# Optimization experiments

Measured on AMD Instinct MI355X. Metric: run time of the kernel, lower is better.

## Reference

```python
import jax, jax.numpy as jnp
import numpy as np

H, W, C = 384, 384, 200
HIDE, CNN_OUT, NCLS = 128, 64, 16
N = H * W
E = 1179648
EPS = 1e-5  # torch BatchNorm eps


def _bn(x, g, b, axes):
    # training-mode batch norm (biased variance), matches torch BN in train mode
    m = x.mean(axes, keepdims=True)
    v = x.var(axes, keepdims=True)
    return (x - m) * jax.lax.rsqrt(v + EPS) * g + b


def _gcn(x, w, bias, src, dst, n):
    # PyG GCNConv: add self loops, symmetric D^-1/2 (A+I) D^-1/2 normalization
    h = x @ w  # [N, out]
    loop = jnp.arange(n, dtype=src.dtype)
    s = jnp.concatenate([src, loop])
    d = jnp.concatenate([dst, loop])
    deg = jax.ops.segment_sum(jnp.ones(s.shape, x.dtype), d, num_segments=n)
    dinv = jnp.where(deg > 0, jax.lax.rsqrt(jnp.maximum(deg, 1.0)) * (deg > 0), 0.0)
    norm = dinv[s] * dinv[d]  # [E+N]
    out = jax.ops.segment_sum(h[s] * norm[:, None], d, num_segments=n)
    return out + bias


def _gnn_layer(x, bn_g, bn_b, w, b, src, dst):
    # F.normalize (row L2) -> BN1d -> GCNConv -> LeakyReLU (dropout off in eval)
    nrm = jnp.linalg.norm(x, axis=1, keepdims=True)
    x = x / jnp.maximum(nrm, 1e-12)
    x = _bn(x, bn_g, bn_b, (0,))
    return jax.nn.leaky_relu(_gcn(x, w, b, src, dst, x.shape[0]))


def setup_inputs() -> dict:
    key = jax.random.key(0)
    ks = jax.random.split(key, 16)
    p = {}
    p["x"] = jax.random.normal(ks[0], (H, W, C), jnp.float32)
    p["edge_index"] = jax.random.randint(ks[1], (2, E), 0, N, jnp.int32)
    # CNN_denoise: BN(C) -> 1x1 conv C->128 -> BN(128) -> 1x1 conv 128->128
    p["dn_bn1_g"] = jnp.ones((C,), jnp.float32); p["dn_bn1_b"] = jnp.zeros((C,), jnp.float32)
    p["dn_w1"] = jax.random.normal(ks[2], (C, HIDE), jnp.float32) * 0.05
    p["dn_b1"] = jnp.zeros((HIDE,), jnp.float32)
    p["dn_bn2_g"] = jnp.ones((HIDE,), jnp.float32); p["dn_bn2_b"] = jnp.zeros((HIDE,), jnp.float32)
    p["dn_w2"] = jax.random.normal(ks[3], (HIDE, HIDE), jnp.float32) * 0.05
    p["dn_b2"] = jnp.zeros((HIDE,), jnp.float32)
    # CNNCONV(128,64,k=5): BN(128) -> point 1x1 128->64 (no bias) -> depthwise 5x5 (bias)
    p["cnn_bn_g"] = jnp.ones((HIDE,), jnp.float32); p["cnn_bn_b"] = jnp.zeros((HIDE,), jnp.float32)
    p["cnn_pw"] = jax.random.normal(ks[4], (HIDE, CNN_OUT), jnp.float32) * 0.05
    p["cnn_dw"] = jax.random.normal(ks[5], (CNN_OUT, 1, 5, 5), jnp.float32) * 0.05
    p["cnn_db"] = jnp.zeros((CNN_OUT,), jnp.float32)
    # GCN branch: GNN(128,128), GNN(128,128), GNN(128,64)
    dims = [(HIDE, HIDE), (HIDE, HIDE), (HIDE, CNN_OUT)]
    for i, (di, do) in enumerate(dims, 1):
        p[f"g{i}_bn_g"] = jnp.ones((di,), jnp.float32)
        p[f"g{i}_bn_b"] = jnp.zeros((di,), jnp.float32)
        p[f"g{i}_w"] = jax.random.normal(ks[5 + i], (di, do), jnp.float32) * 0.05
        p[f"g{i}_b"] = jnp.zeros((do,), jnp.float32)
    p["lin_w"] = jax.random.normal(ks[9], (HIDE, NCLS), jnp.float32) * 0.05
    p["lin_b"] = jnp.zeros((NCLS,), jnp.float32)
    return p


def reference(x, edge_index,
              dn_bn1_g, dn_bn1_b, dn_w1, dn_b1, dn_bn2_g, dn_bn2_b, dn_w2, dn_b2,
              cnn_bn_g, cnn_bn_b, cnn_pw, cnn_dw, cnn_db,
              g1_bn_g, g1_bn_b, g1_w, g1_b,
              g2_bn_g, g2_bn_b, g2_w, g2_b,
              g3_bn_g, g3_bn_b, g3_w, g3_b,
              lin_w, lin_b):
    src, dst = edge_index[0], edge_index[1]
    # CNN_denoise (channel-last; 1x1 convs are matmuls)
    h = _bn(x, dn_bn1_g, dn_bn1_b, (0, 1))
    h = jax.nn.leaky_relu(h @ dn_w1 + dn_b1)
    h = _bn(h, dn_bn2_g, dn_bn2_b, (0, 1))
    clean = jax.nn.leaky_relu(h @ dn_w2 + dn_b2)       # [H,W,128]
    flat = clean.reshape(N, HIDE)
    # CNN branch: BN -> 1x1 -> LeakyReLU -> depthwise 5x5 -> LeakyReLU
    c = _bn(clean, cnn_bn_g, cnn_bn_b, (0, 1))
    c = jax.nn.leaky_relu(c @ cnn_pw)                  # [H,W,64]
    cn = c.transpose(2, 0, 1)[None]                    # [1,64,H,W]
    cn = jax.lax.conv_general_dilated(
        cn, cnn_dw, (1, 1), 'SAME', feature_group_count=CNN_OUT,
        dimension_numbers=('NCHW', 'OIHW', 'NCHW'))
    cn = jax.nn.leaky_relu(cn[0].transpose(1, 2, 0) + cnn_db)
    cnn_res = cn.reshape(N, CNN_OUT)
    # GCN branch (3 layers)
    g = _gnn_layer(flat, g1_bn_g, g1_bn_b, g1_w, g1_b, src, dst)
    g = _gnn_layer(g, g2_bn_g, g2_bn_b, g2_w, g2_b, src, dst)
    g = _gnn_layer(g, g3_bn_g, g3_bn_b, g3_w, g3_b, src, dst)
    y = jnp.concatenate([g, cnn_res], axis=-1) @ lin_w + lin_b
    return jax.nn.softmax(y, axis=-1)
```

## Files before the change

kernel.cpp:

```cpp
#include <hip/hip_runtime.h>
#include <stddef.h>

#define HH 384
#define WW 384
#define CC 200
#define NN 147456
#define EE 1179648
#define HIDE 128
#define COUT 64
#define NCLS 16
#define BN_EPS 1e-5f

#define SREP 16
#define SLOTF (512 * SREP)
#define DBINS 64

#define NBKT 72
#define NPBK 288
#define EPB  4096

using u16 = unsigned short;
typedef __attribute__((ext_vector_type(8))) short short8;
typedef __attribute__((ext_vector_type(4))) float float4v;

__device__ __forceinline__ float b2f(u16 u) {
    union { unsigned int i; float f; } v; v.i = ((unsigned int)u) << 16; return v.f;
}
__device__ __forceinline__ u16 f2b(float f) {
    union { float f; unsigned int i; } v; v.f = f;
    unsigned int x = v.i;
    unsigned int r = (x + 0x7fffu + ((x >> 16) & 1u)) >> 16;
    return (u16)r;
}
__device__ __forceinline__ float lrelu(float v) { return v > 0.f ? v : 0.01f * v; }

__device__ __forceinline__ void gload_lds16(const void* g, void* l) {
    __builtin_amdgcn_global_load_lds(
        (const __attribute__((address_space(1))) void*)g,
        (__attribute__((address_space(3))) void*)l, 16, 0, 0);
}

__global__ void sniff(const u16* __restrict__ x, int* __restrict__ flag) {
    __shared__ int cntS;
    if (threadIdx.x == 0) cntS = 0;
    __syncthreads();
    int c = 0;
    for (int i = 0; i < 8; i++) {
        u16 h = x[threadIdx.x * 8 + i];
        int hb = (h >> 8) & 0x7F;
        if (hb >= 0x3C && hb <= 0x41) c++;
    }
    atomicAdd(&cntS, c);
    __syncthreads();
    if (threadIdx.x == 0) *flag = (cntS < 1536) ? 1 : 0;
}

#define NPAR 27
struct PConv { const void* src[NPAR]; int n[NPAR]; int off[NPAR]; };

__global__ void convert_params(PConv pc, const int* __restrict__ flag,
                               u16* __restrict__ dst) {
    int b = blockIdx.x;
    int n = pc.n[b];
    const void* s = pc.src[b];
    u16* d = dst + pc.off[b];
    int isf = *flag;
    if (isf) {
        const float* sf = (const float*)s;
        for (int i = threadIdx.x; i < n; i += 256) d[i] = f2b(sf[i]);
    } else {
        const u16* sh = (const u16*)s;
        for (int i = threadIdx.x; i < n; i += 256) d[i] = sh[i];
    }
}

__global__ __launch_bounds__(256) void stats200(const void* __restrict__ X,
                                                const int* __restrict__ flag,
                                                float* __restrict__ arena) {
    __shared__ __align__(16) u16 s[128 * 200];
    int t = threadIdx.x;
    int r0 = blockIdx.x * 128;
    if (*flag) {
        const float* Xf = (const float*)X;
        for (int i = t; i < 128 * 25; i += 256) {
            int r = i / 25, kc = i - r * 25;
            const float* p = Xf + (size_t)(r0 + r) * CC + kc * 8;
            float4v a = *(const float4v*)p;
            float4v b = *(const float4v*)(p + 4);
            short8 v;
            #pragma unroll
            for (int j = 0; j < 4; j++) { v[j] = (short)f2b(a[j]); v[4 + j] = (short)f2b(b[j]); }
            *(short8*)&s[r * 200 + kc * 8] = v;
        }
    } else {
        const u16* Xh = (const u16*)X;
        for (int i = t; i < 128 * 25; i += 256) {
            int r = i / 25, kc = i - r * 25;
            *(short8*)&s[r * 200 + kc * 8] =
                *(const short8*)(Xh + (size_t)(r0 + r) * CC + kc * 8);
        }
    }
    __syncthreads();
    if (t < CC) {
        float sum = 0.f, sq = 0.f;
        for (int r = 0; r < 128; r++) {
            float v = b2f(s[r * 200 + t]);
            sum += v; sq += v * v;
        }
        float* rep = arena + (blockIdx.x & (SREP - 1)) * 512;
        atomicAdd(&rep[t], sum);
        atomicAdd(&rep[256 + t], sq);
    }
}

template<int K, int KPAD, int O>
__global__ __launch_bounds__(256) void fold_bn(
        const float* __restrict__ arena, float invN,
        const u16* __restrict__ bng, const u16* __restrict__ bnb,
        const u16* __restrict__ Wsrc, const u16* __restrict__ extrab,
        u16* __restrict__ WT, float* __restrict__ cb) {
    __shared__ float aS[KPAD], sS[KPAD];
    int t = threadIdx.x;
    if (t < KPAD) {
        float a = 0.f, sh = 0.f;
        if (t < K) {
            float sum = 0.f, sq = 0.f;
            #pragma unroll
            for (int r = 0; r < SREP; r++) {
                sum += arena[r * 512 + t];
                sq  += arena[r * 512 + 256 + t];
            }
            float m = sum * invN;
            float var = fmaxf(sq * invN - m * m, 0.f);
            a = b2f(bng[t]) * rsqrtf(var + BN_EPS);
            sh = b2f(bnb[t]) - m * a;
        }
        aS[t] = a; sS[t] = sh;
    }
    __syncthreads();
    int g = t >> 6, l = t & 63;
    int o = blockIdx.x * 4 + g;
    if (o < O) {
        float c = 0.f;
        #pragma unroll
        for (int k = l; k < KPAD; k += 64) {
            float w = (k < K) ? b2f(Wsrc[k * O + o]) : 0.f;
            c += sS[k] * w;
            WT[o * KPAD + k] = f2b(aS[k] * w);
        }
        #pragma unroll
        for (int s = 32; s >= 1; s >>= 1) c += __shfl_down(c, s);
        if (l == 0) cb[o] = c + (extrab ? b2f(extrab[o]) : 0.f);
    }
}

template<int KT, int KSRC, int O, bool LEAKY, bool SCALE, int STATS, bool DUAL>
__global__ __launch_bounds__(256) void gemm_mfma(
        const void* __restrict__ Ap, const u16* __restrict__ WT,
        const float* __restrict__ cb, const float* __restrict__ s1,
        const float* __restrict__ s2, const int* __restrict__ f32p,
        u16* __restrict__ out, float* __restrict__ stA,
        float* __restrict__ stB, float* __restrict__ invn,
        u16* __restrict__ out2, const u16* __restrict__ zpad) {
    constexpr int KPAD = KT * 32;
    constexpr int CHD = KSRC / 8;
    constexpr int ROWCH = ((KT * 4 + 7) / 8) * 8;
    constexpr int ROWE = ROWCH * 8;
    constexpr int LPR = ROWCH;
    constexpr int RPI = 64 / LPR;
    constexpr int NSI = 64 / RPI;
    constexpr int NCT = O / 16;
    constexpr int CPW = NCT / 4;
    __shared__ __align__(16) u16 As[64 * ROWE];
    __shared__ float rS[4][64];
    __shared__ float invS[64];
    __shared__ float sS1[64], sS2[64];
    int tid = threadIdx.x;
    int row0 = blockIdx.x * 64;

    int isf = f32p ? *f32p : 0;
    if (isf) {
        const float* A = (const float*)Ap;
        for (int i = tid; i < 64 * ROWCH; i += 256) {
            int r = i / ROWCH, slot = i - r * ROWCH;
            int chunk = slot ^ (r & 7);
            short8 v = {0, 0, 0, 0, 0, 0, 0, 0};
            if (chunk < CHD) {
                const float* p = A + (size_t)(row0 + r) * KSRC + chunk * 8;
                float4v a = *(const float4v*)p;
                float4v b = *(const float4v*)(p + 4);
                #pragma unroll
                for (int j = 0; j < 4; j++) { v[j] = (short)f2b(a[j]); v[4 + j] = (short)f2b(b[j]); }
            }
            *(short8*)&As[r * ROWE + slot * 8] = v;
        }
    } else {
        const u16* A = (const u16*)Ap;
        int l = tid & 63, wv = tid >> 6;
        int rl0 = l / LPR, cL = l - rl0 * LPR;
        #pragma unroll
        for (int s = 0; s < NSI / 4; s++) {
            int si = wv + s * 4;
            int rL = si * RPI + rl0;
            int chunk = cL ^ (rL & 7);
            const u16* src = (chunk < CHD)
                ? A + (size_t)(row0 + rL) * KSRC + chunk * 8 : zpad;
            gload_lds16(src, (char*)As + si * 1024);
        }
    }
    if (SCALE && tid < 64) { sS1[tid] = s1[row0 + tid]; sS2[tid] = s2[row0 + tid]; }
    __syncthreads();

    int w = tid >> 6, lane = tid & 63, m = lane & 15, q = lane >> 4;
    float4v acc[4][CPW];
    #pragma unroll
    for (int mf = 0; mf < 4; mf++)
        #pragma unroll
        for (int cp = 0; cp < CPW; cp++)
            acc[mf][cp] = (float4v){0.f, 0.f, 0.f, 0.f};

    const u16* Bbp = WT + (size_t)((w * CPW) * 16 + m) * KPAD + q * 8;

    #pragma unroll
    for (int kt = 0; kt < KT; kt++) {
        short8 af[4];
        int slot = (kt * 4 + q) ^ (m & 7);
        #pragma unroll
        for (int mf = 0; mf < 4; mf++)
            af[mf] = *(const short8*)&As[(size_t)(mf * 16 + m) * ROWE + slot * 8];
        #pragma unroll
        for (int cp = 0; cp < CPW; cp++) {
            short8 bf = *(const short8*)(Bbp + (size_t)cp * 16 * KPAD + kt * 32);
            #pragma unroll
            for (int mf = 0; mf < 4; mf++)
                acc[mf][cp] = __builtin_amdgcn_mfma_f32_16x16x32_bf16(
                    af[mf], bf, acc[mf][cp], 0, 0, 0);
        }
    }

    float rp[4][4] = {};
    #pragma unroll
    for (int cp = 0; cp < CPW; cp++) {
        int ct = w * CPW + cp;
        int col = ct * 16 + m;
        float cbv = cb[col];
        #pragma unroll
        for (int mf = 0; mf < 4; mf++) {
            #pragma unroll
            for (int r = 0; r < 4; r++) {
                int rl = mf * 16 + q * 4 + r;
                float x = acc[mf][cp][r];
                if constexpr (DUAL) {
                    if (ct < 8) {
                        x = (x * sS1[rl] + cbv) * sS2[rl];
                        out[(size_t)(row0 + rl) * 128 + col] = f2b(x);
                    } else {
                        x = lrelu(x + cbv);
                        out2[(size_t)(row0 + rl) * 64 + (col - 128)] = f2b(x);
                    }
                } else {
                    if constexpr (SCALE) x = (x * sS1[rl] + cbv) * sS2[rl];
                    else                 x += cbv;
                    if constexpr (LEAKY) x = lrelu(x);
                    out[(size_t)(row0 + rl) * O + col] = f2b(x);
                }
                acc[mf][cp][r] = x;
                if constexpr (STATS == 2) rp[mf][r] += x * x;
            }
        }
    }

    if constexpr (STATS == 2) {
        #pragma unroll
        for (int mf = 0; mf < 4; mf++) {
            #pragma unroll
            for (int r = 0; r < 4; r++) {
                float v = rp[mf][r];
                v += __shfl_xor(v, 1); v += __shfl_xor(v, 2);
                v += __shfl_xor(v, 4); v += __shfl_xor(v, 8);
                if (m == 0) rS[w][mf * 16 + q * 4 + r] = v;
            }
        }
        __syncthreads();
        if (tid < 64) {
            float ss = rS[0][tid] + rS[1][tid] + rS[2][tid] + rS[3][tid];
            float inv = 1.0f / fmaxf(sqrtf(ss), 1e-12f);
            invS[tid] = inv;
            invn[row0 + tid] = inv;
        }
        __syncthreads();
    }

    if constexpr (STATS >= 1) {
        float* stAr = stA + (blockIdx.x & (SREP - 1)) * 512;
        float* stBr = (STATS == 2) ? stB + (blockIdx.x & (SREP - 1)) * 512 : nullptr;
        #pragma unroll
        for (int cp = 0; cp < CPW; cp++) {
            int col = (w * CPW + cp) * 16 + m;
            float cs = 0.f, cq = 0.f, ns = 0.f, nq = 0.f;
            #pragma unroll
            for (int mf = 0; mf < 4; mf++) {
                #pragma unroll
                for (int r = 0; r < 4; r++) {
                    float x = acc[mf][cp][r];
                    cs += x; cq += x * x;
                    if constexpr (STATS == 2) {
                        float nv = x * invS[mf * 16 + q * 4 + r];
                        ns += nv; nq += nv * nv;
                    }
                }
            }
            cs += __shfl_xor(cs, 16); cs += __shfl_xor(cs, 32);
            cq += __shfl_xor(cq, 16); cq += __shfl_xor(cq, 32);
            if constexpr (STATS == 2) {
                ns += __shfl_xor(ns, 16); ns += __shfl_xor(ns, 32);
                nq += __shfl_xor(nq, 16); nq += __shfl_xor(nq, 32);
            }
            if (q == 0) {
                atomicAdd(&stAr[col], cs);
                atomicAdd(&stAr[256 + col], cq);
                if constexpr (STATS == 2) {
                    atomicAdd(&stBr[col], ns);
                    atomicAdd(&stBr[256 + col], nq);
                }
            }
        }
    }
}

__global__ __launch_bounds__(256) void count_bkt(const int* __restrict__ edst,
                                                 int* __restrict__ counts) {
    __shared__ int h[NBKT];
    int t = threadIdx.x, blk = blockIdx.x;
    if (t < NBKT) h[t] = 0;
    __syncthreads();
    int base = blk * EPB;
    for (int i = t; i < EPB; i += 256) {
        unsigned d = (unsigned)edst[base + i];
        if (d < (unsigned)NN) atomicAdd(&h[d >> 11], 1);
    }
    __syncthreads();
    if (t < NBKT) counts[t * NPBK + blk] = h[t];
}

__global__ void scan_bkt(int* __restrict__ counts, int* __restrict__ bbase) {
    __shared__ int bs[NBKT], bb[NBKT];
    int t = threadIdx.x;
    if (t < NBKT) {
        int s = 0;
        for (int i = 0; i < NPBK; i++) s += counts[t * NPBK + i];
        bs[t] = s;
    }
    __syncthreads();
    if (t == 0) {
        int a = 0;
        for (int b = 0; b < NBKT; b++) { bb[b] = a; bbase[b] = a; a += bs[b]; }
        bbase[NBKT] = a;
    }
    __syncthreads();
    if (t < NBKT) {
        int run = bb[t];
        for (int i = 0; i < NPBK; i++) {
            int c = counts[t * NPBK + i];
            counts[t * NPBK + i] = run;
            run += c;
        }
    }
}

__global__ __launch_bounds__(256) void part_bkt(const int* __restrict__ esrc,
                                                const int* __restrict__ edst,
                                                const int* __restrict__ counts,
                                                int2* __restrict__ bpair) {
    __shared__ int2 buf[EPB];
    __shared__ int lcnt[NBKT], lbase[NBKT], gbase[NBKT];
    int t = threadIdx.x, blk = blockIdx.x;
    if (t < NBKT) lcnt[t] = 0;
    __syncthreads();
    int base = blk * EPB;
    int dv[16], sv[16];
    #pragma unroll
    for (int j = 0; j < 16; j++) {
        dv[j] = edst[base + t + j * 256];
        sv[j] = esrc[base + t + j * 256];
        unsigned ud = (unsigned)dv[j];
        if (ud < (unsigned)NN) atomicAdd(&lcnt[ud >> 11], 1);
    }
    __syncthreads();
    if (t == 0) {
        int a = 0;
        for (int b = 0; b < NBKT; b++) { lbase[b] = a; a += lcnt[b]; }
    }
    __syncthreads();
    if (t < NBKT) { gbase[t] = counts[t * NPBK + blk]; lcnt[t] = 0; }
    __syncthreads();
    #pragma unroll
    for (int j = 0; j < 16; j++) {
        unsigned ud = (unsigned)dv[j];
        if (ud < (unsigned)NN) {
            int b = ud >> 11;
            int p = lbase[b] + atomicAdd(&lcnt[b], 1);
            int2 e; e.x = sv[j]; e.y = (int)ud;
            buf[p] = e;
        }
    }
    __syncthreads();
    int tot = lbase[NBKT - 1] + lcnt[NBKT - 1];
    for (int i = t; i < tot; i += 256) {
        int2 p = buf[i];
        int b = ((unsigned)p.y) >> 11;
        bpair[gbase[b] + (i - lbase[b])] = p;
    }
}

__global__ __launch_bounds__(256) void csr_build(const int2* __restrict__ bpair,
                                                 const int* __restrict__ bbase,
                                                 int* __restrict__ offv,
                                                 int* __restrict__ csr) {
    __shared__ int cntL[2048];
    __shared__ int exL[2048];
    __shared__ int tsum[256];
    int b = blockIdx.x, t = threadIdx.x;
    int e0 = bbase[b], e1 = bbase[b + 1];
    int n0 = b << 11;
    for (int i = t; i < 2048; i += 256) cntL[i] = 0;
    __syncthreads();
    for (int k = e0 + t; k < e1; k += 256) {
        int2 p = bpair[k];
        atomicAdd(&cntL[p.y & 2047], 1);
    }
    __syncthreads();
    int s = 0;
    #pragma unroll
    for (int j = 0; j < 8; j++) s += cntL[t * 8 + j];
    tsum[t] = s;
    __syncthreads();
    for (int o = 1; o < 256; o <<= 1) {
        int x = (t >= o) ? tsum[t - o] : 0;
        __syncthreads();
        tsum[t] += x;
        __syncthreads();
    }
    int run = tsum[t] - s;
    #pragma unroll
    for (int j = 0; j < 8; j++) { int c = cntL[t * 8 + j]; exL[t * 8 + j] = run; run += c; }
    __syncthreads();
    for (int i = t; i < 2048; i += 256) offv[n0 + i] = e0 + exL[i];
    if (b == NBKT - 1 && t == 0) offv[NN] = e1;
    for (int i = t; i < 2048; i += 256) cntL[i] = 0;
    __syncthreads();
    for (int k = e0 + t; k < e1; k += 256) {
        int2 p = bpair[k];
        int l = p.y & 2047;
        int pos = e0 + exL[l] + atomicAdd(&cntL[l], 1);
        csr[pos] = p.x;
    }
}

__global__ void mkdinv_deghist(const int* __restrict__ offv,
                               float* __restrict__ dinv, int* __restrict__ dbin) {
    __shared__ int h[DBINS];
    int t = threadIdx.x;
    if (t < DBINS) h[t] = 0;
    __syncthreads();
    int i = blockIdx.x * 256 + t;
    int dg = offv[i + 1] - offv[i];
    if (dg < 0) dg = 0;
    dinv[i] = rsqrtf((float)dg + 1.0f);
    int dc = dg > DBINS - 1 ? DBINS - 1 : dg;
    atomicAdd(&h[dc], 1);
    __syncthreads();
    if (t < DBINS) atomicAdd(&dbin[t], h[t]);
}
__global__ void deg_scan(const int* __restrict__ dbin, int* __restrict__ dbase) {
    if (threadIdx.x == 0) {
        int a = 0;
        for (int b = DBINS - 1; b >= 0; b--) { dbase[b] = a; a += dbin[b]; }
    }
}
__global__ void deg_scatter(const int* __restrict__ offv, int* __restrict__ dbase,
                            int* __restrict__ perm) {
    __shared__ int h[DBINS], base[DBINS];
    int t = threadIdx.x;
    if (t < DBINS) h[t] = 0;
    __syncthreads();
    int i = blockIdx.x * 256 + t;
    int dg = offv[i + 1] - offv[i];
    if (dg < 0) dg = 0; if (dg > DBINS - 1) dg = DBINS - 1;
    atomicAdd(&h[dg], 1);
    __syncthreads();
    if (t < DBINS) { base[t] = atomicAdd(&dbase[t], h[t]); h[t] = 0; }
    __syncthreads();
    int lp = atomicAdd(&h[dg], 1);
    perm[base[dg] + lp] = i;
}

template<int O, int STATS, int GRP>
__global__ __launch_bounds__(256) void aggregate(
        const u16* __restrict__ h2, const int* __restrict__ offv,
        const int* __restrict__ csr, const float* __restrict__ dinv,
        const u16* __restrict__ gb, u16* __restrict__ outp,
        float* __restrict__ stA, float* __restrict__ invn,
        const int* __restrict__ perm) {
    constexpr int CH = O / 8;
    constexpr int NPB = 256 / CH;
    __shared__ float colS[O], colQ[O];
    int t = threadIdx.x;
    if (STATS && t < O) { colS[t] = 0.f; colQ[t] = 0.f; }
    int local = t / CH, c = t % CH;
    size_t cof = (size_t)c * 8;
    const u16* hb = h2 + cof;
    short8 gv = *(const short8*)(gb + cof);
    float sreg[8] = {0.f, 0.f, 0.f, 0.f, 0.f, 0.f, 0.f, 0.f};
    float qreg[8] = {0.f, 0.f, 0.f, 0.f, 0.f, 0.f, 0.f, 0.f};

    #pragma unroll
    for (int g = 0; g < GRP; g++) {
        int pos = blockIdx.x * (NPB * GRP) + g * NPB + local;
        int d = perm[pos];
        float acc[8];
        short8 selfv = *(const short8*)(hb + (size_t)d * O);
        #pragma unroll
        for (int j = 0; j < 8; j++) acc[j] = b2f((u16)selfv[j]);
        int e0 = offv[d], e1 = offv[d + 1];
        if (e0 < 0) e0 = 0;
        if (e1 > EE) e1 = EE;
        int k = e0;
        for (; k + 8 <= e1; k += 8) {
            unsigned i0 = (unsigned)csr[k],     i1 = (unsigned)csr[k + 1];
            unsigned i2 = (unsigned)csr[k + 2], i3 = (unsigned)csr[k + 3];
            unsigned i4 = (unsigned)csr[k + 4], i5 = (unsigned)csr[k + 5];
            unsigned i6 = (unsigned)csr[k + 6], i7 = (unsigned)csr[k + 7];
            short8 v0 = *(const short8*)(hb + (size_t)i0 * O);
            short8 v1 = *(const short8*)(hb + (size_t)i1 * O);
            short8 v2 = *(const short8*)(hb + (size_t)i2 * O);
            short8 v3 = *(const short8*)(hb + (size_t)i3 * O);
            short8 v4 = *(const short8*)(hb + (size_t)i4 * O);
            short8 v5 = *(const short8*)(hb + (size_t)i5 * O);
            short8 v6 = *(const short8*)(hb + (size_t)i6 * O);
            short8 v7 = *(const short8*)(hb + (size_t)i7 * O);
            #pragma unroll
            for (int j = 0; j < 8; j++)
                acc[j] += ((b2f((u16)v0[j]) + b2f((u16)v1[j])) +
                           (b2f((u16)v2[j]) + b2f((u16)v3[j]))) +
                          ((b2f((u16)v4[j]) + b2f((u16)v5[j])) +
                           (b2f((u16)v6[j]) + b2f((u16)v7[j])));
        }
        if (k + 4 <= e1) {
            unsigned i0 = (unsigned)csr[k],     i1 = (unsigned)csr[k + 1];
            unsigned i2 = (unsigned)csr[k + 2], i3 = (unsigned)csr[k + 3];
            short8 v0 = *(const short8*)(hb + (size_t)i0 * O);
            short8 v1 = *(const short8*)(hb + (size_t)i1 * O);
            short8 v2 = *(const short8*)(hb + (size_t)i2 * O);
            short8 v3 = *(const short8*)(hb + (size_t)i3 * O);
            #pragma unroll
            for (int j = 0; j < 8; j++)
                acc[j] += (b2f((u16)v0[j]) + b2f((u16)v1[j])) +
                          (b2f((u16)v2[j]) + b2f((u16)v3[j]));
            k += 4;
        }
        if (k + 2 <= e1) {
            unsigned i0 = (unsigned)csr[k], i1 = (unsigned)csr[k + 1];
            short8 v0 = *(const short8*)(hb + (size_t)i0 * O);
            short8 v1 = *(const short8*)(hb + (size_t)i1 * O);
            #pragma unroll
            for (int j = 0; j < 8; j++)
                acc[j] += b2f((u16)v0[j]) + b2f((u16)v1[j]);
            k += 2;
        }
        if (k < e1) {
            unsigned i0 = (unsigned)csr[k];
            short8 v0 = *(const short8*)(hb + (size_t)i0 * O);
            #pragma unroll
            for (int j = 0; j < 8; j++) acc[j] += b2f((u16)v0[j]);
        }
        float dd = dinv[d];
        float outv[8];
        short8 res;
        #pragma unroll
        for (int j = 0; j < 8; j++) {
            outv[j] = lrelu(dd * acc[j] + b2f((u16)gv[j]));
            res[j] = (short)f2b(outv[j]);
        }
        *(short8*)(outp + (size_t)d * O + cof) = res;

        if constexpr (STATS) {
            float ss = 0.f;
            #pragma unroll
            for (int j = 0; j < 8; j++) ss += outv[j] * outv[j];
            ss += __shfl_xor(ss, 1); ss += __shfl_xor(ss, 2);
            ss += __shfl_xor(ss, 4); ss += __shfl_xor(ss, 8);
            float inv = 1.0f / fmaxf(sqrtf(ss), 1e-12f);
            if (c == 0) invn[d] = inv;
            #pragma unroll
            for (int j = 0; j < 8; j++) {
                float nv = outv[j] * inv;
                sreg[j] += nv; qreg[j] += nv * nv;
            }
        }
    }

    if constexpr (STATS) {
        __syncthreads();
        #pragma unroll
        for (int j = 0; j < 8; j++) {
            float s = sreg[j];
            s += __shfl_xor(s, 16); s += __shfl_xor(s, 32);
            float qq = qreg[j];
            qq += __shfl_xor(qq, 16); qq += __shfl_xor(qq, 32);
            if ((t & 63) < 16) {
                atomicAdd(&colS[c * 8 + j], s);
                atomicAdd(&colQ[c * 8 + j], qq);
            }
        }
        __syncthreads();
        if (t < O) {
            float* rep = stA + (blockIdx.x & (SREP - 1)) * 512;
            atomicAdd(&rep[t], colS[t]);
            atomicAdd(&rep[256 + t], colQ[t]);
        }
    }
}

__global__ __launch_bounds__(256) void final_fused(
        const u16* __restrict__ g3, const u16* __restrict__ cpre,
        const u16* __restrict__ dwW, const u16* __restrict__ db,
        const u16* __restrict__ lw, const u16* __restrict__ lb,
        const int* __restrict__ flag, void* __restrict__ outp) {
    __shared__ __align__(16) u16 tile[400 * 72];
    __shared__ __align__(16) u16 wT[25 * 64];
    __shared__ __align__(16) u16 wL[2048];
    __shared__ float bDW[64];
    __shared__ float bL[16];
    int t = threadIdx.x;
    int tx = blockIdx.x % 24, ty = blockIdx.x / 24;
    int x0 = tx * 16 - 2, y0 = ty * 16 - 2;
    for (int i = t; i < 1600; i += 256) {
        int f = i / 25, tap = i - f * 25;
        wT[tap * 64 + f] = dwW[i];
    }
    for (int i = t; i < 2048; i += 256) wL[i] = lw[i];
    if (t < 64) bDW[t] = b2f(db[t]);
    if (t < 16) bL[t] = b2f(lb[t]);
    for (int u = t; u < 3200; u += 256) {
        int pix = u >> 3, c8 = u & 7;
        int gy = y0 + pix / 20, gx = x0 + pix % 20;
        short8 v = {0, 0, 0, 0, 0, 0, 0, 0};
        if (gy >= 0 && gy < HH && gx >= 0 && gx < WW)
            v = *(const short8*)(cpre + ((size_t)(gy * WW + gx)) * 64 + c8 * 8);
        *(short8*)&tile[pix * 72 + c8 * 8] = v;
    }
    __syncthreads();

    int px = t & 15, py = t >> 4;
    int node = (ty * 16 + py) * WW + tx * 16 + px;
    float y[16];
    #pragma unroll
    for (int o = 0; o < 16; o++) y[o] = bL[o];

    const u16* g3p = g3 + (size_t)node * 64;
    for (int c8 = 0; c8 < 8; c8++) {
        short8 gvv = *(const short8*)(g3p + c8 * 8);
        #pragma unroll
        for (int j = 0; j < 8; j++) {
            float g = b2f((u16)gvv[j]);
            const short8 w0 = *(const short8*)&wL[(c8 * 8 + j) * 16];
            const short8 w1 = *(const short8*)&wL[(c8 * 8 + j) * 16 + 8];
            #pragma unroll
            for (int o = 0; o < 8; o++) {
                y[o]     += g * b2f((u16)w0[o]);
                y[o + 8] += g * b2f((u16)w1[o]);
            }
        }
    }
    for (int c8 = 0; c8 < 8; c8++) {
        float acc[8] = {0.f, 0.f, 0.f, 0.f, 0.f, 0.f, 0.f, 0.f};
        #pragma unroll
        for (int dy = 0; dy < 5; dy++) {
            int rbase = ((py + dy) * 20 + px) * 72 + c8 * 8;
            #pragma unroll
            for (int dx = 0; dx < 5; dx++) {
                short8 v  = *(const short8*)&tile[rbase + dx * 72];
                short8 wv = *(const short8*)&wT[(dy * 5 + dx) * 64 + c8 * 8];
                #pragma unroll
                for (int j = 0; j < 8; j++)
                    acc[j] += b2f((u16)v[j]) * b2f((u16)wv[j]);
            }
        }
        #pragma unroll
        for (int j = 0; j < 8; j++) {
            float cv = lrelu(acc[j] + bDW[c8 * 8 + j]);
            int f = 64 + c8 * 8 + j;
            const short8 w0 = *(const short8*)&wL[f * 16];
            const short8 w1 = *(const short8*)&wL[f * 16 + 8];
            #pragma unroll
            for (int o = 0; o < 8; o++) {
                y[o]     += cv * b2f((u16)w0[o]);
                y[o + 8] += cv * b2f((u16)w1[o]);
            }
        }
    }
    float mx = y[0];
    #pragma unroll
    for (int o = 1; o < 16; o++) mx = fmaxf(mx, y[o]);
    float sum = 0.f;
    #pragma unroll
    for (int o = 0; o < 16; o++) { y[o] = __expf(y[o] - mx); sum += y[o]; }
    float inv = 1.0f / fmaxf(sum, 1e-30f);
    if (*flag) {
        float* of = (float*)outp;
        #pragma unroll
        for (int o = 0; o < 16; o++) of[(size_t)node * 16 + o] = y[o] * inv;
    } else {
        u16* oh = (u16*)outp;
        #pragma unroll
        for (int o = 0; o < 16; o++) oh[(size_t)node * 16 + o] = f2b(y[o] * inv);
    }
}

extern "C" void kernel_launch(void* const* d_in, const int* in_sizes, int n_in,
                              void* d_out, int out_size, void* d_ws, size_t ws_size,
                              hipStream_t stream) {
    const void* X   = d_in[0];
    const int* EIDX = (const int*)d_in[1];
    const int* esrc = EIDX;
    const int* edst = EIDX + EE;

    char* ws = (char*)d_ws;
    size_t off = 0;
    auto alloc = [&](size_t sz) -> char* {
        size_t szr = (sz + 255) & ~(size_t)255;
        char* p;
        if (off + szr <= ws_size) { p = ws + off; off += szr; }
        else { p = ws; }
        return p;
    };

    int*   dflag   = (int*)alloc(256);
    static const int pidx[NPAR] = {2,3,4,5,6,7,8,9,10,11,12,13,14,
                                   15,16,17,18,19,20,21,22,23,24,25,26,27,28};
    static const int pn[NPAR]   = {200,200,25600,128,128,128,16384,128,
                                   128,128,8192,1600,64,
                                   128,128,16384,128,
                                   128,128,16384,128,
                                   128,128,8192,64,
                                   2048,16};
    u16* parena = (u16*)alloc(100352 * 2);
    PConv pc;
    {
        int po = 0;
        for (int i = 0; i < NPAR; i++) {
            pc.src[i] = d_in[pidx[i]];
            pc.n[i] = pn[i];
            pc.off[i] = po;
            po += (pn[i] + 15) & ~15;
        }
    }
    const u16* DN1G = parena + pc.off[0];
    const u16* DN1B = parena + pc.off[1];
    const u16* DNW1 = parena + pc.off[2];
    const u16* DNB1 = parena + pc.off[3];
    const u16* DN2G = parena + pc.off[4];
    const u16* DN2B = parena + pc.off[5];
    const u16* DNW2 = parena + pc.off[6];
    const u16* DNB2 = parena + pc.off[7];
    const u16* CBNG = parena + pc.off[8];
    const u16* CBNB = parena + pc.off[9];
    const u16* CPW  = parena + pc.off[10];
    const u16* CDW  = parena + pc.off[11];
    const u16* CDB  = parena + pc.off[12];
    const u16* G1G  = parena + pc.off[13];
    const u16* G1B  = parena + pc.off[14];
    const u16* G1W  = parena + pc.off[15];
    const u16* G1BI = parena + pc.off[16];
    const u16* G2G  = parena + pc.off[17];
    const u16* G2B  = parena + pc.off[18];
    const u16* G2W  = parena + pc.off[19];
    const u16* G2BI = parena + pc.off[20];
    const u16* G3G  = parena + pc.off[21];
    const u16* G3B  = parena + pc.off[22];
    const u16* G3W  = parena + pc.off[23];
    const u16* G3BI = parena + pc.off[24];
    const u16* LINW = parena + pc.off[25];
    const u16* LINB = parena + pc.off[26];

    float* arena   = (float*)alloc((size_t)6 * SLOTF * 4);
    int*   dbin    = (int*)alloc(DBINS * 4);
    u16*   zpad    = (u16*)alloc(256);
    int*   counts  = (int*)alloc((size_t)NBKT * NPBK * 4);
    int*   bbase   = (int*)alloc((NBKT + 1) * 4);
    int2*  bpair   = (int2*)alloc((size_t)EE * 8);
    int*   offv    = (int*)alloc((size_t)(NN + 1) * 4);
    int*   dbase   = (int*)alloc(DBINS * 4);
    int*   perm    = (int*)alloc((size_t)NN * 4);
    float* dinvp   = (float*)alloc((size_t)NN * 4);
    float* invnorm = (float*)alloc((size_t)NN * 4);
    u16*   W1T     = (u16*)alloc(128 * 224 * 2);
    u16*   W2T     = (u16*)alloc(128 * 128 * 2);
    u16*   WgT     = (u16*)alloc(192 * 128 * 2);
    float* cb1     = (float*)alloc(128 * 4);
    float* cb2     = (float*)alloc(128 * 4);
    float* cbg     = (float*)alloc(192 * 4);
    int*   csr     = (int*)alloc((size_t)EE * 4);
    u16*   cbuf    = (u16*)alloc((size_t)NN * 64 * 2);
    u16*   big1    = (u16*)alloc((size_t)NN * 128 * 2);
    u16*   big2    = (u16*)alloc((size_t)NN * 128 * 2);

    const float invN = 1.0f / (float)NN;
    size_t zsz = (size_t)((char*)zpad + 256 - (char*)arena);
    size_t zcap = ((char*)arena >= ws && (size_t)((char*)arena - ws) < ws_size)
                      ? ws_size - (size_t)((char*)arena - ws) : 0;
    if (zsz > zcap) zsz = zcap;
    hipMemsetAsync(arena, 0, zsz, stream);

    sniff<<<1, 256, 0, stream>>>((const u16*)X, dflag);
    convert_params<<<NPAR, 256, 0, stream>>>(pc, dflag, parena);

    count_bkt<<<NPBK, 256, 0, stream>>>(edst, counts);
    scan_bkt<<<1, 128, 0, stream>>>(counts, bbase);
    part_bkt<<<NPBK, 256, 0, stream>>>(esrc, edst, counts, bpair);
    csr_build<<<NBKT, 256, 0, stream>>>(bpair, bbase, offv, csr);
    mkdinv_deghist<<<NN / 256, 256, 0, stream>>>(offv, dinvp, dbin);
    deg_scan<<<1, 64, 0, stream>>>(dbin, dbase);
    deg_scatter<<<NN / 256, 256, 0, stream>>>(offv, dbase, perm);

    stats200<<<1152, 256, 0, stream>>>(X, dflag, arena + 0 * SLOTF);
    fold_bn<200, 224, 128><<<32, 256, 0, stream>>>(arena + 0 * SLOTF, invN, DN1G, DN1B, DNW1, DNB1, W1T, cb1);
    gemm_mfma<7, 200, 128, true, false, 1, false><<<NN / 64, 256, 0, stream>>>(
        X, W1T, cb1, nullptr, nullptr, dflag, big1, arena + 1 * SLOTF, nullptr, nullptr, nullptr, zpad);
    fold_bn<128, 128, 128><<<32, 256, 0, stream>>>(arena + 1 * SLOTF, invN, DN2G, DN2B, DNW2, DNB2, W2T, cb2);
    gemm_mfma<4, 128, 128, true, false, 2, false><<<NN / 64, 256, 0, stream>>>(
        big1, W2T, cb2, nullptr, nullptr, nullptr, big2, arena + 2 * SLOTF, arena + 3 * SLOTF, invnorm, nullptr, zpad);

    fold_bn<128, 128, 128><<<32, 256, 0, stream>>>(arena + 3 * SLOTF, invN, G1G, G1B, G1W, nullptr, WgT, cbg);
    fold_bn<128, 128, 64><<<16, 256, 0, stream>>>(arena + 2 * SLOTF, invN, CBNG, CBNB, CPW, nullptr,
                                                  WgT + 128 * 128, cbg + 128);
    gemm_mfma<4, 128, 192, false, true, 0, true><<<NN / 64, 256, 0, stream>>>(
        big2, WgT, cbg, invnorm, dinvp, nullptr, big1, nullptr, nullptr, nullptr, cbuf, zpad);
    aggregate<128, 1, 4><<<NN / 64, 256, 0, stream>>>(
        big1, offv, csr, dinvp, G1BI, big2, arena + 4 * SLOTF, invnorm, perm);

    fold_bn<128, 128, 128><<<32, 256, 0, stream>>>(arena + 4 * SLOTF, invN, G2G, G2B, G2W, nullptr, WgT, cbg);
    gemm_mfma<4, 128, 128, false, true, 0, false><<<NN / 64, 256, 0, stream>>>(
        big2, WgT, cbg, invnorm, dinvp, nullptr, big1, nullptr, nullptr, nullptr, nullptr, zpad);
    aggregate<128, 1, 4><<<NN / 64, 256, 0, stream>>>(
        big1, offv, csr, dinvp, G2BI, big2, arena + 5 * SLOTF, invnorm, perm);

    fold_bn<128, 128, 64><<<16, 256, 0, stream>>>(arena + 5 * SLOTF, invN, G3G, G3B, G3W, nullptr, WgT, cbg);
    gemm_mfma<4, 128, 64, false, true, 0, false><<<NN / 64, 256, 0, stream>>>(
        big2, WgT, cbg, invnorm, dinvp, nullptr, big1, nullptr, nullptr, nullptr, nullptr, zpad);
    aggregate<64, 0, 1><<<NN / 32, 256, 0, stream>>>(
        big1, offv, csr, dinvp, G3BI, big2, nullptr, nullptr, perm);

    final_fused<<<576, 256, 0, stream>>>(big2, cbuf, CDW, CDB, LINW, LINB, dflag, d_out);

    (void)in_sizes; (void)n_in; (void)out_size;
}
```

Before: 745.8 us.

## Cache bf16 input in stats pass, fold degree pass into CSR build, pair fold_bn launches

The stats pass now writes the bf16-converted input to a new workspace buffer. The first GEMM then loads it through the async global-to-LDS path instead of re-reading and converting fp32. The separate dinv/degree-histogram kernel is merged into csr_build, using the per-node counts already in shared memory. Two fold_bn launches are merged into one kernel. Together these cut fp32 re-reads and remove two launches, at the cost of an extra ~59MB bf16 write and a larger workspace.

```diff
diff --git a/kernel.cpp b/kernel.cpp
--- a/kernel.cpp
+++ b/kernel.cpp
@@ -76,7 +76,8 @@
 
 __global__ __launch_bounds__(256) void stats200(const void* __restrict__ X,
                                                 const int* __restrict__ flag,
-                                                float* __restrict__ arena) {
+                                                float* __restrict__ arena,
+                                                u16* __restrict__ Xbf) {
     __shared__ __align__(16) u16 s[128 * 200];
     int t = threadIdx.x;
     int r0 = blockIdx.x * 128;
@@ -92,6 +93,11 @@
             for (int j = 0; j < 4; j++) { v[j] = (short)f2b(a[j]); v[4 + j] = (short)f2b(b[j]); }
             *(short8*)&s[r * 200 + kc * 8] = v;
         }
+        for (int i = t; i < 128 * 25; i += 256) {
+            int r = i / 25, kc = i - r * 25;
+            *(short8*)(Xbf + (size_t)(r0 + r) * CC + kc * 8) =
+                *(const short8*)&s[r * 200 + kc * 8];
+        }
     } else {
         const u16* Xh = (const u16*)X;
         for (int i = t; i < 128 * 25; i += 256) {
@@ -114,11 +120,11 @@
 }
 
 template<int K, int KPAD, int O>
-__global__ __launch_bounds__(256) void fold_bn(
+__device__ __forceinline__ void fold_bn_body(
         const float* __restrict__ arena, float invN,
         const u16* __restrict__ bng, const u16* __restrict__ bnb,
         const u16* __restrict__ Wsrc, const u16* __restrict__ extrab,
-        u16* __restrict__ WT, float* __restrict__ cb) {
+        u16* __restrict__ WT, float* __restrict__ cb, int blk) {
     __shared__ float aS[KPAD], sS[KPAD];
     int t = threadIdx.x;
     if (t < KPAD) {
@@ -139,7 +145,7 @@
     }
     __syncthreads();
     int g = t >> 6, l = t & 63;
-    int o = blockIdx.x * 4 + g;
+    int o = blk * 4 + g;
     if (o < O) {
         float c = 0.f;
         #pragma unroll
@@ -154,9 +160,35 @@
     }
 }
 
+template<int K, int KPAD, int O>
+__global__ __launch_bounds__(256) void fold_bn(
+        const float* __restrict__ arena, float invN,
+        const u16* __restrict__ bng, const u16* __restrict__ bnb,
+        const u16* __restrict__ Wsrc, const u16* __restrict__ extrab,
+        u16* __restrict__ WT, float* __restrict__ cb) {
+    fold_bn_body<K, KPAD, O>(arena, invN, bng, bnb, Wsrc, extrab, WT, cb,
+                             blockIdx.x);
+}
+
+__global__ __launch_bounds__(256) void fold_bn_pair(
+        const float* __restrict__ arenaA, const float* __restrict__ arenaB,
+        float invN,
+        const u16* __restrict__ bngA, const u16* __restrict__ bnbA,
+        const u16* __restrict__ WA, u16* __restrict__ WTA, float* __restrict__ cbA,
+        const u16* __restrict__ bngB, const u16* __restrict__ bnbB,
+        const u16* __restrict__ WB, u16* __restrict__ WTB, float* __restrict__ cbB) {
+    if (blockIdx.x < 32)
+        fold_bn_body<128, 128, 128>(arenaA, invN, bngA, bnbA, WA, nullptr,
+                                    WTA, cbA, blockIdx.x);
+    else
+        fold_bn_body<128, 128, 64>(arenaB, invN, bngB, bnbB, WB, nullptr,
+                                   WTB, cbB, blockIdx.x - 32);
+}
+
 template<int KT, int KSRC, int O, bool LEAKY, bool SCALE, int STATS, bool DUAL>
 __global__ __launch_bounds__(256) void gemm_mfma(
-        const void* __restrict__ Ap, const u16* __restrict__ WT,
+        const void* __restrict__ Ap, const u16* __restrict__ Abf,
+        const u16* __restrict__ WT,
         const float* __restrict__ cb, const float* __restrict__ s1,
         const float* __restrict__ s2, const int* __restrict__ f32p,
         u16* __restrict__ out, float* __restrict__ stA,
@@ -179,23 +211,8 @@
     int row0 = blockIdx.x * 64;
 
     int isf = f32p ? *f32p : 0;
-    if (isf) {
-        const float* A = (const float*)Ap;
-        for (int i = tid; i < 64 * ROWCH; i += 256) {
-            int r = i / ROWCH, slot = i - r * ROWCH;
-            int chunk = slot ^ (r & 7);
-            short8 v = {0, 0, 0, 0, 0, 0, 0, 0};
-            if (chunk < CHD) {
-                const float* p = A + (size_t)(row0 + r) * KSRC + chunk * 8;
-                float4v a = *(const float4v*)p;
-                float4v b = *(const float4v*)(p + 4);
-                #pragma unroll
-                for (int j = 0; j < 4; j++) { v[j] = (short)f2b(a[j]); v[4 + j] = (short)f2b(b[j]); }
-            }
-            *(short8*)&As[r * ROWE + slot * 8] = v;
-        }
-    } else {
-        const u16* A = (const u16*)Ap;
+    const u16* A = isf ? Abf : (const u16*)Ap;
+    {
         int l = tid & 63, wv = tid >> 6;
         int rl0 = l / LPR, cL = l - rl0 * LPR;
         #pragma unroll
@@ -416,10 +433,13 @@
 __global__ __launch_bounds__(256) void csr_build(const int2* __restrict__ bpair,
                                                  const int* __restrict__ bbase,
                                                  int* __restrict__ offv,
-                                                 int* __restrict__ csr) {
+                                                 int* __restrict__ csr,
+                                                 float* __restrict__ dinv,
+                                                 int* __restrict__ dbin) {
     __shared__ int cntL[2048];
     __shared__ int exL[2048];
     __shared__ int tsum[256];
+    __shared__ int hh[DBINS];
     int b = blockIdx.x, t = threadIdx.x;
     int e0 = bbase[b], e1 = bbase[b + 1];
     int n0 = b << 11;
@@ -448,6 +468,7 @@
     for (int i = t; i < 2048; i += 256) offv[n0 + i] = e0 + exL[i];
     if (b == NBKT - 1 && t == 0) offv[NN] = e1;
     for (int i = t; i < 2048; i += 256) cntL[i] = 0;
+    if (t < DBINS) hh[t] = 0;
     __syncthreads();
     for (int k = e0 + t; k < e1; k += 256) {
         int2 p = bpair[k];
@@ -455,23 +476,17 @@
         int pos = e0 + exL[l] + atomicAdd(&cntL[l], 1);
         csr[pos] = p.x;
     }
-}
-
-__global__ void mkdinv_deghist(const int* __restrict__ offv,
-                               float* __restrict__ dinv, int* __restrict__ dbin) {
-    __shared__ int h[DBINS];
-    int t = threadIdx.x;
-    if (t < DBINS) h[t] = 0;
-    __syncthreads();
-    int i = blockIdx.x * 256 + t;
-    int dg = offv[i + 1] - offv[i];
-    if (dg < 0) dg = 0;
-    dinv[i] = rsqrtf((float)dg + 1.0f);
-    int dc = dg > DBINS - 1 ? DBINS - 1 : dg;
-    atomicAdd(&h[dc], 1);
-    __syncthreads();
-    if (t < DBINS) atomicAdd(&dbin[t], h[t]);
-}
+    __syncthreads();
+    for (int i = t; i < 2048; i += 256) {
+        int dg = cntL[i];
+        dinv[n0 + i] = rsqrtf((float)dg + 1.0f);
+        int dc = dg > DBINS - 1 ? DBINS - 1 : dg;
+        atomicAdd(&hh[dc], 1);
+    }
+    __syncthreads();
+    if (t < DBINS) atomicAdd(&dbin[t], hh[t]);
+}
+
 __global__ void deg_scan(const int* __restrict__ dbin, int* __restrict__ dbase) {
     if (threadIdx.x == 0) {
         int a = 0;
@@ -802,6 +817,7 @@
     float* cb2     = (float*)alloc(128 * 4);
     float* cbg     = (float*)alloc(192 * 4);
     int*   csr     = (int*)alloc((size_t)EE * 4);
+    u16*   Xbf     = (u16*)alloc((size_t)NN * CC * 2);
     u16*   cbuf    = (u16*)alloc((size_t)NN * 64 * 2);
     u16*   big1    = (u16*)alloc((size_t)NN * 128 * 2);
     u16*   big2    = (u16*)alloc((size_t)NN * 128 * 2);
@@ -819,36 +835,36 @@
     count_bkt<<<NPBK, 256, 0, stream>>>(edst, counts);
     scan_bkt<<<1, 128, 0, stream>>>(counts, bbase);
     part_bkt<<<NPBK, 256, 0, stream>>>(esrc, edst, counts, bpair);
-    csr_build<<<NBKT, 256, 0, stream>>>(bpair, bbase, offv, csr);
-    mkdinv_deghist<<<NN / 256, 256, 0, stream>>>(offv, dinvp, dbin);
+    csr_build<<<NBKT, 256, 0, stream>>>(bpair, bbase, offv, csr, dinvp, dbin);
     deg_scan<<<1, 64, 0, stream>>>(dbin, dbase);
     deg_scatter<<<NN / 256, 256, 0, stream>>>(offv, dbase, perm);
 
-    stats200<<<1152, 256, 0, stream>>>(X, dflag, arena + 0 * SLOTF);
+    stats200<<<1152, 256, 0, stream>>>(X, dflag, arena + 0 * SLOTF, Xbf);
     fold_bn<200, 224, 128><<<32, 256, 0, stream>>>(arena + 0 * SLOTF, invN, DN1G, DN1B, DNW1, DNB1, W1T, cb1);
     gemm_mfma<7, 200, 128, true, false, 1, false><<<NN / 64, 256, 0, stream>>>(
-        X, W1T, cb1, nullptr, nullptr, dflag, big1, arena + 1 * SLOTF, nullptr, nullptr, nullptr, zpad);
+        X, Xbf, W1T, cb1, nullptr, nullptr, dflag, big1, arena + 1 * SLOTF, nullptr, nullptr, nullptr, zpad);
     fold_bn<128, 128, 128><<<32, 256, 0, stream>>>(arena + 1 * SLOTF, invN, DN2G, DN2B, DNW2, DNB2, W2T, cb2);
     gemm_mfma<4, 128, 128, true, false, 2, false><<<NN / 64, 256, 0, stream>>>(
-        big1, W2T, cb2, nullptr, nullptr, nullptr, big2, arena + 2 * SLOTF, arena + 3 * SLOTF, invnorm, nullptr, zpad);
-
-    fold_bn<128, 128, 128><<<32, 256, 0, stream>>>(arena + 3 * SLOTF, invN, G1G, G1B, G1W, nullptr, WgT, cbg);
-    fold_bn<128, 128, 64><<<16, 256, 0, stream>>>(arena + 2 * SLOTF, invN, CBNG, CBNB, CPW, nullptr,
-                                                  WgT + 128 * 128, cbg + 128);
+        big1, nullptr, W2T, cb2, nullptr, nullptr, nullptr, big2, arena + 2 * SLOTF, arena + 3 * SLOTF, invnorm, nullptr, zpad);
+
+    fold_bn_pair<<<48, 256, 0, stream>>>(
+        arena + 3 * SLOTF, arena + 2 * SLOTF, invN,
+        G1G, G1B, G1W, WgT, cbg,
+        CBNG, CBNB, CPW, WgT + 128 * 128, cbg + 128);
     gemm_mfma<4, 128, 192, false, true, 0, true><<<NN / 64, 256, 0, stream>>>(
-        big2, WgT, cbg, invnorm, dinvp, nullptr, big1, nullptr, nullptr, nullptr, cbuf, zpad);
+        big2, nullptr, WgT, cbg, invnorm, dinvp, nullptr, big1, nullptr, nullptr, nullptr, cbuf, zpad);
     aggregate<128, 1, 4><<<NN / 64, 256, 0, stream>>>(
         big1, offv, csr, dinvp, G1BI, big2, arena + 4 * SLOTF, invnorm, perm);
 
     fold_bn<128, 128, 128><<<32, 256, 0, stream>>>(arena + 4 * SLOTF, invN, G2G, G2B, G2W, nullptr, WgT, cbg);
     gemm_mfma<4, 128, 128, false, true, 0, false><<<NN / 64, 256, 0, stream>>>(
-        big2, WgT, cbg, invnorm, dinvp, nullptr, big1, nullptr, nullptr, nullptr, nullptr, zpad);
+        big2, nullptr, WgT, cbg, invnorm, dinvp, nullptr, big1, nullptr, nullptr, nullptr, nullptr, zpad);
     aggregate<128, 1, 4><<<NN / 64, 256, 0, stream>>>(
         big1, offv, csr, dinvp, G2BI, big2, arena + 5 * SLOTF, invnorm, perm);
 
     fold_bn<128, 128, 64><<<16, 256, 0, stream>>>(arena + 5 * SLOTF, invN, G3G, G3B, G3W, nullptr, WgT, cbg);
     gemm_mfma<4, 128, 64, false, true, 0, false><<<NN / 64, 256, 0, stream>>>(
-        big2, WgT, cbg, invnorm, dinvp, nullptr, big1, nullptr, nullptr, nullptr, nullptr, zpad);
+        big2, nullptr, WgT, cbg, invnorm, dinvp, nullptr, big1, nullptr, nullptr, nullptr, nullptr, zpad);
     aggregate<64, 0, 1><<<NN / 32, 256, 0, stream>>>(
         big1, offv, csr, dinvp, G3BI, big2, nullptr, nullptr, perm);
 
```

Result: no change. 740.5 us (-0.7%).
